# Kernel optimization log

Hardware: AMD Instinct MI355X
Metric: run time of the kernel (lower is better)

## Reference

```python
import jax, jax.numpy as jnp
import numpy as np

D_MODEL = 1024
NUM_HEADS = 16
D_K = D_MODEL // NUM_HEADS
THETA = 10000.0
SEQ = 4096
BATCH = 1


def _rope(x, pos):
    # x: [..., S, d_k]; pos: [S]
    inv_freq = 1.0 / (THETA ** (jnp.arange(0, D_K, 2, dtype=jnp.float32) / D_K))  # [d_k/2]
    freqs = pos.astype(jnp.float32)[:, None] * inv_freq[None, :]  # [S, d_k/2]
    cos = jnp.cos(freqs)
    sin = jnp.sin(freqs)
    x_even = x[..., ::2]
    x_odd = x[..., 1::2]
    out1 = cos * x_even - sin * x_odd
    out2 = sin * x_even + cos * x_odd
    # interleave: stack on new last axis then flatten (matches torch.stack(...,-1).flatten(-2))
    out = jnp.stack([out1, out2], axis=-1).reshape(x.shape)
    return out


def setup_inputs() -> dict:
    key = jax.random.key(0)
    ks = jax.random.split(key, 5)
    std = (2.0 / (D_MODEL + D_MODEL)) ** 0.5
    x = jax.random.normal(ks[0], (BATCH, SEQ, D_MODEL), dtype=jnp.float32)
    wq = jax.random.normal(ks[1], (D_MODEL, D_MODEL), dtype=jnp.float32) * std
    wk = jax.random.normal(ks[2], (D_MODEL, D_MODEL), dtype=jnp.float32) * std
    wv = jax.random.normal(ks[3], (D_MODEL, D_MODEL), dtype=jnp.float32) * std
    wo = jax.random.normal(ks[4], (D_MODEL, D_MODEL), dtype=jnp.float32) * std
    return {"x": x, "wq": wq, "wk": wk, "wv": wv, "wo": wo}


def reference(x, wq, wk, wv, wo):
    b, s, d = x.shape
    # projections: y = x @ W.T  (weight stored [out, in])
    q = jnp.einsum('bsd,od->bso', x, wq)
    k = jnp.einsum('bsd,od->bso', x, wk)
    v = jnp.einsum('bsd,od->bso', x, wv)
    # split heads -> [b, h, s, d_k]
    q = q.reshape(b, s, NUM_HEADS, D_K).transpose(0, 2, 1, 3)
    k = k.reshape(b, s, NUM_HEADS, D_K).transpose(0, 2, 1, 3)
    v = v.reshape(b, s, NUM_HEADS, D_K).transpose(0, 2, 1, 3)
    pos = jnp.arange(s)
    q = _rope(q, pos)
    k = _rope(k, pos)
    scores = jnp.einsum('bhqd,bhkd->bhqk', q, k) / (D_K ** 0.5)
    causal = jnp.tril(jnp.ones((s, s), dtype=bool))
    scores = jnp.where(causal, scores, -jnp.inf)
    attn = jax.nn.softmax(scores, axis=-1)
    out = jnp.einsum('bhqk,bhkd->bhqd', attn, v)
    out = out.transpose(0, 2, 1, 3).reshape(b, s, d)
    out = jnp.einsum('bsd,od->bso', out, wo)
    return out
```

## Files before the change

kernel.cpp:

```cpp
#include <hip/hip_runtime.h>
#include <math.h>

#define SEQ    4096
#define DMODEL 1024
#define NHEADS 16
#define DK     64

typedef unsigned short u16;
typedef short bh8 __attribute__((ext_vector_type(8)));
typedef float f4  __attribute__((ext_vector_type(4)));

__device__ __forceinline__ u16 f2b(float f) {
    union { float f; unsigned u; } v; v.f = f;
    unsigned u = v.u;
    return (u16)((u + 0x7FFFu + ((u >> 16) & 1u)) >> 16);
}
__device__ __forceinline__ unsigned pk2(float a, float b) {
    union { float f; unsigned u; } ua, ub; ua.f = a; ub.f = b;
    return (ua.u >> 16) | (ub.u & 0xFFFF0000u);
}

__global__ void cvt_all_kernel(const float* __restrict__ x,
                               const float* __restrict__ wq, const float* __restrict__ wk,
                               const float* __restrict__ wv, const float* __restrict__ wo,
                               u16* __restrict__ xb, u16* __restrict__ wb)
{
    const int NX = SEQ * DMODEL / 8;
    const int NW = DMODEL * DMODEL / 8;
    int i = blockIdx.x * blockDim.x + threadIdx.x;
    if (i >= NX + 4 * NW) return;
    const float* src; u16* dst; int j;
    if (i < NX) { src = x; dst = xb; j = i; }
    else {
        int k = i - NX;
        int wsel = k >> 17;
        j = k & (NW - 1);
        src = (wsel == 0) ? wq : (wsel == 1) ? wk : (wsel == 2) ? wv : wo;
        dst = wb + (size_t)wsel * DMODEL * DMODEL;
    }
    const float4* p = (const float4*)src + (size_t)j * 2;
    float4 a = p[0], b = p[1];
    __align__(16) u16 r[8] = { f2b(a.x), f2b(a.y), f2b(a.z), f2b(a.w),
                               f2b(b.x), f2b(b.y), f2b(b.z), f2b(b.w) };
    *(uint4*)(dst + (size_t)j * 8) = *(const uint4*)r;
}

template<int MODE>
__global__ __launch_bounds__(256) void gemm_bt(
    const u16* __restrict__ A, const u16* __restrict__ B,
    void* __restrict__ out, u16* __restrict__ Qh, u16* __restrict__ Kh,
    u16* __restrict__ Vt, int M, int N, int K)
{
    constexpr int BN = (MODE == 0) ? 64 : 128;
    constexpr int NJ = BN / 32;

    __shared__ __align__(16) u16 As[128 * 32];
    __shared__ __align__(16) u16 Bs[BN * 32];

    const int t    = threadIdx.x;
    const int w    = t >> 6, lane = t & 63;
    const int quad = lane >> 4, l16 = lane & 15;
    const int wm   = w >> 1,  wn  = w & 1;
    const int m0   = blockIdx.y * 128, n0 = blockIdx.x * BN;
    const int lr   = lane >> 2;
    const int lc   = (lane & 3) * 8;

    f4 acc[4][NJ];
#pragma unroll
    for (int i = 0; i < 4; ++i)
#pragma unroll
        for (int j = 0; j < NJ; ++j) { f4 z = {0.f,0.f,0.f,0.f}; acc[i][j] = z; }

    const int c0 = 2 * w, c1 = 2 * w + 1;

    for (int k0 = 0; k0 < K; k0 += 32) {
        __builtin_amdgcn_global_load_lds(
            (const __attribute__((address_space(1))) unsigned int*)(A + (size_t)(m0 + c0*16 + lr)*K + k0 + lc),
            (__attribute__((address_space(3))) unsigned int*)(As + c0*512), 16, 0, 0);
        __builtin_amdgcn_global_load_lds(
            (const __attribute__((address_space(1))) unsigned int*)(A + (size_t)(m0 + c1*16 + lr)*K + k0 + lc),
            (__attribute__((address_space(3))) unsigned int*)(As + c1*512), 16, 0, 0);
        if (MODE == 0) {
            __builtin_amdgcn_global_load_lds(
                (const __attribute__((address_space(1))) unsigned int*)(B + (size_t)(n0 + w*16 + lr)*K + k0 + lc),
                (__attribute__((address_space(3))) unsigned int*)(Bs + w*512), 16, 0, 0);
        } else {
            __builtin_amdgcn_global_load_lds(
                (const __attribute__((address_space(1))) unsigned int*)(B + (size_t)(n0 + c0*16 + lr)*K + k0 + lc),
                (__attribute__((address_space(3))) unsigned int*)(Bs + c0*512), 16, 0, 0);
            __builtin_amdgcn_global_load_lds(
                (const __attribute__((address_space(1))) unsigned int*)(B + (size_t)(n0 + c1*16 + lr)*K + k0 + lc),
                (__attribute__((address_space(3))) unsigned int*)(Bs + c1*512), 16, 0, 0);
        }
        __syncthreads();

        bh8 af[4], bf_[NJ];
#pragma unroll
        for (int i = 0; i < 4; ++i)
            af[i] = *(const bh8*)&As[(wm*64 + i*16 + l16)*32 + quad*8];
#pragma unroll
        for (int j = 0; j < NJ; ++j)
            bf_[j] = *(const bh8*)&Bs[(wn*(BN/2) + j*16 + l16)*32 + quad*8];
#pragma unroll
        for (int i = 0; i < 4; ++i)
#pragma unroll
            for (int j = 0; j < NJ; ++j)
                acc[i][j] = __builtin_amdgcn_mfma_f32_16x16x32_bf16(af[i], bf_[j], acc[i][j], 0, 0, 0);
        __syncthreads();
    }

    if (MODE == 0) {
#pragma unroll
        for (int i = 0; i < 4; ++i) {
            const int row = m0 + wm*64 + i*16 + quad*4;
#pragma unroll
            for (int j = 0; j < NJ; ++j) {
                const int col = n0 + wn*(BN/2) + j*16 + l16;
#pragma unroll
                for (int r = 0; r < 4; ++r)
                    ((float*)out)[(size_t)(row + r) * N + col] = acc[i][j][r];
            }
        }
    } else {
        const int sect  = n0 >> 10;
        const int cbase = (n0 & 1023) + wn * 64;
        const int hh    = cbase >> 6;
        if (sect < 2) {
            u16* dst = (sect == 0) ? Qh : Kh;
            const float qscl = (sect == 0) ? 0.18033688011112042f : 1.0f;
#pragma unroll
            for (int j = 0; j < NJ; ++j) {
                const int d = j * 16 + l16;
                const float invf2 = exp2f((float)(d & ~1) * (-13.287712379549449f / 64.0f))
                                    * 0.15915494309189535f;
#pragma unroll
                for (int i = 0; i < 4; ++i) {
                    const int srow0 = m0 + wm*64 + i*16 + quad*4;
#pragma unroll
                    for (int r = 0; r < 4; ++r) {
                        float own = acc[i][j][r];
                        float oth = __shfl_xor(own, 1);
                        float rev = (float)(srow0 + r) * invf2;
                        rev -= floorf(rev);
                        float sn = __builtin_amdgcn_sinf(rev);
                        float cs = __builtin_amdgcn_cosf(rev);
                        float xe = (l16 & 1) ? oth : own;
                        float xo = (l16 & 1) ? own : oth;
                        float val = (l16 & 1) ? (sn * xe + cs * xo)
                                              : (cs * xe - sn * xo);
                        dst[((size_t)hh * SEQ + srow0 + r) * DK + d] = f2b(val * qscl);
                    }
                }
            }
        } else {
#pragma unroll
            for (int j = 0; j < NJ; ++j) {
                const int d = j * 16 + l16;
#pragma unroll
                for (int i = 0; i < 4; ++i) {
                    const int srow0 = m0 + wm*64 + i*16 + quad*4;
                    __align__(8) u16 pk[4];
#pragma unroll
                    for (int r = 0; r < 4; ++r) pk[r] = f2b(acc[i][j][r]);
                    *(unsigned long long*)&Vt[((size_t)hh * DK + d) * SEQ + srow0] =
                        *(const unsigned long long*)pk;
                }
            }
        }
    }
}

__global__ __launch_bounds__(512) void attn_mfma_kernel(
    const u16* __restrict__ Qh, const u16* __restrict__ Kh,
    const u16* __restrict__ Vt, u16* __restrict__ ctx)
{
    __shared__ __align__(16) u16 Ks[2][64 * 64];
    __shared__ __align__(16) u16 Vs[2][64 * 64];

    const int h    = blockIdx.y;
    const int bx   = blockIdx.x;
    const int t    = threadIdx.x;
    const int w    = t >> 6, lane = t & 63;
    const int wl   = w & 3, hh = w >> 2;
    const int quad = lane >> 4, l16 = lane & 15;

    const u16* Kbase = Kh + (size_t)h * SEQ * DK;
    const u16* Vbase = Vt + (size_t)h * DK * SEQ;

    const int sA = ((quad       ^ (l16 & 7)) * 8);
    const int sB = (((4 + quad) ^ (l16 & 7)) * 8);

    int koff;
    {
        const int r7 = lane >> 3;
        const int s  = lane & 7;
        koff = (w * 8 + r7) * DK + ((s ^ r7) * 8);
    }

    const int vd  = t >> 3;
    const int vs0 = (t & 7) * 8;
    int wv0, wv1;
    {
        const int vd7 = vd & 7;
        const int c2  = t & 7;
        const int kbp = c2 >> 2, cm = c2 & 3;
        const int qa  = (2 * cm) & 3;
        const int qb  = (2 * cm + 1) & 3;
        const int jhi = cm >> 1;
        wv0 = vd * 64 + ((kbp * 4 + qa) ^ vd7) * 8 + jhi * 4;
        wv1 = vd * 64 + ((kbp * 4 + qb) ^ vd7) * 8 + jhi * 4;
    }

    for (int part = 0; part < 2; ++part) {
        const int qt = part ? (63 - bx) : bx;
        const int q0 = qt * 64;
        const int nk = qt + 1;

        bh8 qa0, qa1;
        {
            const u16* qrow = Qh + ((size_t)h * SEQ + q0 + wl * 16 + l16) * DK;
            qa0 = *(const bh8*)(qrow + quad * 8);
            qa1 = *(const bh8*)(qrow + 32 + quad * 8);
        }

        f4 o[4];
        float lsum = 0.f;
#pragma unroll
        for (int j = 0; j < 4; ++j) { f4 z = {0.f,0.f,0.f,0.f}; o[j] = z; }

        __syncthreads();
        __builtin_amdgcn_global_load_lds(
            (const __attribute__((address_space(1))) unsigned int*)(Kbase + koff),
            (__attribute__((address_space(3))) unsigned int*)&Ks[0][w * 512],
            16, 0, 0);
        {
            uint4 v0 = *(const uint4*)&Vbase[(size_t)vd * SEQ + vs0];
            uint2 c;
            c.x = v0.x; c.y = v0.y; *(uint2*)&Vs[0][wv0] = c;
            c.x = v0.z; c.y = v0.w; *(uint2*)&Vs[0][wv1] = c;
        }
        __syncthreads();

        int b = 0;
        uint4 v0n;
        for (int kt = 0; kt < nk; ++kt) {
            const bool have_next = (kt + 1 < nk);

            if (have_next) {
                const int kn = (kt + 1) * 64;
                __builtin_amdgcn_global_load_lds(
                    (const __attribute__((address_space(1))) unsigned int*)(Kbase + (size_t)kn * DK + koff),
                    (__attribute__((address_space(3))) unsigned int*)&Ks[b ^ 1][w * 512],
                    16, 0, 0);
                v0n = *(const uint4*)&Vbase[(size_t)vd * SEQ + kn + vs0];
            }

            float sv[2][4];
            __builtin_amdgcn_s_setprio(1);
#pragma unroll
            for (int kk = 0; kk < 2; ++kk) {
                const int kb = hh * 2 + kk;
                const int rb = (kb * 16 + l16) * 64;
                bh8 kf0 = *(const bh8*)&Ks[b][rb + sA];
                bh8 kf1 = *(const bh8*)&Ks[b][rb + sB];
                f4 a = {0.f,0.f,0.f,0.f};
                a = __builtin_amdgcn_mfma_f32_16x16x32_bf16(kf0, qa0, a, 0, 0, 0);
                a = __builtin_amdgcn_mfma_f32_16x16x32_bf16(kf1, qa1, a, 0, 0, 0);
#pragma unroll
                for (int r = 0; r < 4; ++r) sv[kk][r] = a[r];
            }
            __builtin_amdgcn_s_setprio(0);
            if (kt == qt) {
#pragma unroll
                for (int kk = 0; kk < 2; ++kk)
#pragma unroll
                    for (int r = 0; r < 4; ++r)
                        if ((hh * 2 + kk) * 16 + quad * 4 + r > wl * 16 + l16)
                            sv[kk][r] = -1.0e30f;
            }

            float p[2][4];
#pragma unroll
            for (int kk = 0; kk < 2; ++kk) {
                p[kk][0] = exp2f(sv[kk][0]); p[kk][1] = exp2f(sv[kk][1]);
                p[kk][2] = exp2f(sv[kk][2]); p[kk][3] = exp2f(sv[kk][3]);
                lsum += (p[kk][0] + p[kk][1]) + (p[kk][2] + p[kk][3]);
            }

            {
                union { unsigned u[4]; bh8 v; } pc;
                pc.u[0] = pk2(p[0][0], p[0][1]);
                pc.u[1] = pk2(p[0][2], p[0][3]);
                pc.u[2] = pk2(p[1][0], p[1][1]);
                pc.u[3] = pk2(p[1][2], p[1][3]);
                const bh8 pb = pc.v;
                const int sc = hh ? sB : sA;
                __builtin_amdgcn_s_setprio(1);
#pragma unroll
                for (int jd = 0; jd < 4; ++jd) {
                    bh8 va = *(const bh8*)&Vs[b][(jd * 16 + l16) * 64 + sc];
                    o[jd] = __builtin_amdgcn_mfma_f32_16x16x32_bf16(va, pb, o[jd], 0, 0, 0);
                }
                __builtin_amdgcn_s_setprio(0);
            }

            if (have_next) {
                uint2 c;
                c.x = v0n.x; c.y = v0n.y; *(uint2*)&Vs[b ^ 1][wv0] = c;
                c.x = v0n.z; c.y = v0n.w; *(uint2*)&Vs[b ^ 1][wv1] = c;
                __syncthreads();
                b ^= 1;
            }
        }

        lsum += __shfl_xor(lsum, 16);
        lsum += __shfl_xor(lsum, 32);
        __syncthreads();
        float* scr = ((w & 2) ? (float*)Vs : (float*)Ks)
                     + ((w & 1) * 64 + lane) * 20;
        if (hh) {
#pragma unroll
            for (int jd = 0; jd < 4; ++jd) *(f4*)(scr + jd * 4) = o[jd];
            scr[16] = lsum;
        }
        __syncthreads();
        if (!hh) {
#pragma unroll
            for (int jd = 0; jd < 4; ++jd) {
                f4 po = *(const f4*)(scr + jd * 4);
#pragma unroll
                for (int r = 0; r < 4; ++r) o[jd][r] += po[r];
            }
            lsum += scr[16];
            const float linv = 1.f / lsum;
            const size_t rowbase = (size_t)(q0 + wl * 16 + l16) * DMODEL + h * DK;
#pragma unroll
            for (int jd = 0; jd < 4; ++jd) {
                unsigned lo = (unsigned)f2b(o[jd][0] * linv) | ((unsigned)f2b(o[jd][1] * linv) << 16);
                unsigned hi = (unsigned)f2b(o[jd][2] * linv) | ((unsigned)f2b(o[jd][3] * linv) << 16);
                uint2 pkd; pkd.x = lo; pkd.y = hi;
                *(uint2*)&ctx[rowbase + jd * 16 + quad * 4] = pkd;
            }
        }
    }
}

extern "C" void kernel_launch(void* const* d_in, const int* in_sizes, int n_in,
                              void* d_out, int out_size, void* d_ws, size_t ws_size,
                              hipStream_t stream)
{
    const float* x  = (const float*)d_in[0];
    const float* wq = (const float*)d_in[1];
    const float* wk = (const float*)d_in[2];
    const float* wv = (const float*)d_in[3];
    const float* wo = (const float*)d_in[4];
    float* out = (float*)d_out;

    char* ws = (char*)d_ws;
    const size_t MB = 1u << 20;
    u16* xb   = (u16*)(ws);
    u16* wqkv = (u16*)(ws + 8  * MB);
    u16* wob  = (u16*)(ws + 14 * MB);
    u16* Qh   = (u16*)(ws + 16 * MB);
    u16* Kh   = (u16*)(ws + 24 * MB);
    u16* Vtb  = (u16*)(ws + 32 * MB);
    u16* ctxb = (u16*)(ws + 40 * MB);

    const int NCVT = SEQ * DMODEL / 8 + 4 * (DMODEL * DMODEL / 8);
    cvt_all_kernel<<<NCVT / 256, 256, 0, stream>>>(x, wq, wk, wv, wo, xb, wqkv);

    dim3 gqkv(3 * DMODEL / 128, SEQ / 128);
    gemm_bt<2><<<gqkv, 256, 0, stream>>>(xb, wqkv, nullptr, Qh, Kh, Vtb,
                                         SEQ, 3 * DMODEL, DMODEL);

    attn_mfma_kernel<<<dim3(32, NHEADS), 512, 0, stream>>>(Qh, Kh, Vtb, ctxb);

    dim3 go(DMODEL / 64, SEQ / 128);
    gemm_bt<0><<<go, 256, 0, stream>>>(ctxb, wob, out, nullptr, nullptr, nullptr,
                                       SEQ, DMODEL, DMODEL);
}
```

Measured before the change: 225.4 us.

## Precompute RoPE table and load K fragments directly into registers

Adds a small kernel that builds a cos/sin table per (position, frequency), which the QKV GEMM epilogue now reads instead of evaluating sin/cos inline. The attention kernel stops staging K tiles through LDS with global_load_lds. Each wave instead loads its K MFMA fragments straight from global memory into registers, double-buffered across iterations, and the merge scratch moves to a dedicated LDS array. This removes transcendental work from the epilogue and LDS traffic for K. In exchange it adds an extra launch and table reads, and brings uncoalesced, duplicated per-wave global loads of K.

```diff
diff --git a/kernel.cpp b/kernel.cpp
--- a/kernel.cpp
+++ b/kernel.cpp
@@ -45,11 +45,25 @@
     *(uint4*)(dst + (size_t)j * 8) = *(const uint4*)r;
 }
 
+__global__ void rope_build_kernel(float2* __restrict__ tab)
+{
+    int i = blockIdx.x * blockDim.x + threadIdx.x;
+    int s = i >> 5, f = i & 31;
+    float invf2 = exp2f((float)(2 * f) * (-13.287712379549449f / 64.0f))
+                  * 0.15915494309189535f;
+    float rev = (float)s * invf2;
+    rev -= floorf(rev);
+    float2 cs;
+    cs.x = __builtin_amdgcn_cosf(rev);
+    cs.y = __builtin_amdgcn_sinf(rev);
+    tab[i] = cs;
+}
+
 template<int MODE>
 __global__ __launch_bounds__(256) void gemm_bt(
     const u16* __restrict__ A, const u16* __restrict__ B,
     void* __restrict__ out, u16* __restrict__ Qh, u16* __restrict__ Kh,
-    u16* __restrict__ Vt, int M, int N, int K)
+    u16* __restrict__ Vt, const float2* __restrict__ rope, int M, int N, int K)
 {
     constexpr int BN = (MODE == 0) ? 64 : 128;
     constexpr int NJ = BN / 32;
@@ -130,9 +144,8 @@
             const float qscl = (sect == 0) ? 0.18033688011112042f : 1.0f;
 #pragma unroll
             for (int j = 0; j < NJ; ++j) {
-                const int d = j * 16 + l16;
-                const float invf2 = exp2f((float)(d & ~1) * (-13.287712379549449f / 64.0f))
-                                    * 0.15915494309189535f;
+                const int d  = j * 16 + l16;
+                const int fr = j * 8 + (l16 >> 1);
 #pragma unroll
                 for (int i = 0; i < 4; ++i) {
                     const int srow0 = m0 + wm*64 + i*16 + quad*4;
@@ -140,10 +153,8 @@
                     for (int r = 0; r < 4; ++r) {
                         float own = acc[i][j][r];
                         float oth = __shfl_xor(own, 1);
-                        float rev = (float)(srow0 + r) * invf2;
-                        rev -= floorf(rev);
-                        float sn = __builtin_amdgcn_sinf(rev);
-                        float cs = __builtin_amdgcn_cosf(rev);
+                        float2 cssn = rope[(size_t)(srow0 + r) * 32 + fr];
+                        const float cs = cssn.x, sn = cssn.y;
                         float xe = (l16 & 1) ? oth : own;
                         float xo = (l16 & 1) ? own : oth;
                         float val = (l16 & 1) ? (sn * xe + cs * xo)
@@ -174,8 +185,8 @@
     const u16* __restrict__ Qh, const u16* __restrict__ Kh,
     const u16* __restrict__ Vt, u16* __restrict__ ctx)
 {
-    __shared__ __align__(16) u16 Ks[2][64 * 64];
     __shared__ __align__(16) u16 Vs[2][64 * 64];
+    __shared__ __align__(16) float mscr[4 * 64 * 20];
 
     const int h    = blockIdx.y;
     const int bx   = blockIdx.x;
@@ -190,12 +201,13 @@
     const int sA = ((quad       ^ (l16 & 7)) * 8);
     const int sB = (((4 + quad) ^ (l16 & 7)) * 8);
 
-    int koff;
-    {
-        const int r7 = lane >> 3;
-        const int s  = lane & 7;
-        koff = (w * 8 + r7) * DK + ((s ^ r7) * 8);
-    }
+    const u16* kp[4];
+#pragma unroll
+    for (int kk = 0; kk < 2; ++kk)
+#pragma unroll
+        for (int hf = 0; hf < 2; ++hf)
+            kp[kk * 2 + hf] = Kbase + (size_t)((hh * 2 + kk) * 16 + l16) * DK
+                              + hf * 32 + quad * 8;
 
     const int vd  = t >> 3;
     const int vs0 = (t & 7) * 8;
@@ -228,11 +240,11 @@
 #pragma unroll
         for (int j = 0; j < 4; ++j) { f4 z = {0.f,0.f,0.f,0.f}; o[j] = z; }
 
-        __syncthreads();
-        __builtin_amdgcn_global_load_lds(
-            (const __attribute__((address_space(1))) unsigned int*)(Kbase + koff),
-            (__attribute__((address_space(3))) unsigned int*)&Ks[0][w * 512],
-            16, 0, 0);
+        bh8 kc0 = *(const bh8*)kp[0];
+        bh8 kc1 = *(const bh8*)kp[1];
+        bh8 kc2 = *(const bh8*)kp[2];
+        bh8 kc3 = *(const bh8*)kp[3];
+        __syncthreads();
         {
             uint4 v0 = *(const uint4*)&Vbase[(size_t)vd * SEQ + vs0];
             uint2 c;
@@ -242,32 +254,33 @@
         __syncthreads();
 
         int b = 0;
-        uint4 v0n;
         for (int kt = 0; kt < nk; ++kt) {
             const bool have_next = (kt + 1 < nk);
 
+            bh8 kn0, kn1, kn2, kn3;
+            uint4 v0n;
             if (have_next) {
-                const int kn = (kt + 1) * 64;
-                __builtin_amdgcn_global_load_lds(
-                    (const __attribute__((address_space(1))) unsigned int*)(Kbase + (size_t)kn * DK + koff),
-                    (__attribute__((address_space(3))) unsigned int*)&Ks[b ^ 1][w * 512],
-                    16, 0, 0);
-                v0n = *(const uint4*)&Vbase[(size_t)vd * SEQ + kn + vs0];
+                const size_t ko = (size_t)(kt + 1) * 64 * DK;
+                kn0 = *(const bh8*)(kp[0] + ko);
+                kn1 = *(const bh8*)(kp[1] + ko);
+                kn2 = *(const bh8*)(kp[2] + ko);
+                kn3 = *(const bh8*)(kp[3] + ko);
+                v0n = *(const uint4*)&Vbase[(size_t)vd * SEQ + (kt + 1) * 64 + vs0];
             }
 
             float sv[2][4];
             __builtin_amdgcn_s_setprio(1);
-#pragma unroll
-            for (int kk = 0; kk < 2; ++kk) {
-                const int kb = hh * 2 + kk;
-                const int rb = (kb * 16 + l16) * 64;
-                bh8 kf0 = *(const bh8*)&Ks[b][rb + sA];
-                bh8 kf1 = *(const bh8*)&Ks[b][rb + sB];
+            {
                 f4 a = {0.f,0.f,0.f,0.f};
-                a = __builtin_amdgcn_mfma_f32_16x16x32_bf16(kf0, qa0, a, 0, 0, 0);
-                a = __builtin_amdgcn_mfma_f32_16x16x32_bf16(kf1, qa1, a, 0, 0, 0);
-#pragma unroll
-                for (int r = 0; r < 4; ++r) sv[kk][r] = a[r];
+                a = __builtin_amdgcn_mfma_f32_16x16x32_bf16(kc0, qa0, a, 0, 0, 0);
+                a = __builtin_amdgcn_mfma_f32_16x16x32_bf16(kc1, qa1, a, 0, 0, 0);
+#pragma unroll
+                for (int r = 0; r < 4; ++r) sv[0][r] = a[r];
+                f4 c = {0.f,0.f,0.f,0.f};
+                c = __builtin_amdgcn_mfma_f32_16x16x32_bf16(kc2, qa0, c, 0, 0, 0);
+                c = __builtin_amdgcn_mfma_f32_16x16x32_bf16(kc3, qa1, c, 0, 0, 0);
+#pragma unroll
+                for (int r = 0; r < 4; ++r) sv[1][r] = c[r];
             }
             __builtin_amdgcn_s_setprio(0);
             if (kt == qt) {
@@ -308,6 +321,7 @@
                 uint2 c;
                 c.x = v0n.x; c.y = v0n.y; *(uint2*)&Vs[b ^ 1][wv0] = c;
                 c.x = v0n.z; c.y = v0n.w; *(uint2*)&Vs[b ^ 1][wv1] = c;
+                kc0 = kn0; kc1 = kn1; kc2 = kn2; kc3 = kn3;
                 __syncthreads();
                 b ^= 1;
             }
@@ -315,9 +329,7 @@
 
         lsum += __shfl_xor(lsum, 16);
         lsum += __shfl_xor(lsum, 32);
-        __syncthreads();
-        float* scr = ((w & 2) ? (float*)Vs : (float*)Ks)
-                     + ((w & 1) * 64 + lane) * 20;
+        float* scr = mscr + (((w & 3) * 64) + lane) * 20;
         if (hh) {
 #pragma unroll
             for (int jd = 0; jd < 4; ++jd) *(f4*)(scr + jd * 4) = o[jd];
@@ -365,17 +377,20 @@
     u16* Kh   = (u16*)(ws + 24 * MB);
     u16* Vtb  = (u16*)(ws + 32 * MB);
     u16* ctxb = (u16*)(ws + 40 * MB);
+    float2* rope = (float2*)(ws + 40 * MB);
+
+    rope_build_kernel<<<(SEQ * 32) / 256, 256, 0, stream>>>(rope);
 
     const int NCVT = SEQ * DMODEL / 8 + 4 * (DMODEL * DMODEL / 8);
     cvt_all_kernel<<<NCVT / 256, 256, 0, stream>>>(x, wq, wk, wv, wo, xb, wqkv);
 
     dim3 gqkv(3 * DMODEL / 128, SEQ / 128);
-    gemm_bt<2><<<gqkv, 256, 0, stream>>>(xb, wqkv, nullptr, Qh, Kh, Vtb,
+    gemm_bt<2><<<gqkv, 256, 0, stream>>>(xb, wqkv, nullptr, Qh, Kh, Vtb, rope,
                                          SEQ, 3 * DMODEL, DMODEL);
 
     attn_mfma_kernel<<<dim3(32, NHEADS), 512, 0, stream>>>(Qh, Kh, Vtb, ctxb);
 
     dim3 go(DMODEL / 64, SEQ / 128);
     gemm_bt<0><<<go, 256, 0, stream>>>(ctxb, wob, out, nullptr, nullptr, nullptr,
-                                       SEQ, DMODEL, DMODEL);
-}
+                                       nullptr, SEQ, DMODEL, DMODEL);
+}
```

Result: slower. 285.3 us (+26.5%).
